# Kernel optimization log

Measured on AMD Instinct MI355X. Metric: run time of the kernel, lower is better.

Reference implementation:

```python
import jax, jax.numpy as jnp
import numpy as np

B, P, N, E, H, D = 8, 1000, 1000, 128, 8, 16  # batch, pomo, nodes, embed, heads, qkv_dim
SQRT_E = float(np.sqrt(E))
CLIP = 10.0
INV_SQRT_D = 1.0 / float(np.sqrt(D))


def _heads(x):
    # [b, n, H*D] -> [b, H, n, D]
    b, n, _ = x.shape
    return x.reshape(b, n, H, D).transpose(0, 2, 1, 3)


def _mha(q, k, v, ninf_mask):
    # q: [b,H,P,D], k/v: [b,H,N,D], ninf_mask: [b,P,N]
    score = jnp.einsum('bhnd,bhsd->bhns', q, k) * INV_SQRT_D
    score = score + ninf_mask[:, None, :, :]
    w = jax.nn.softmax(score, axis=-1)
    out = jnp.einsum('bhns,bhsd->bhnd', w, v)
    return out.transpose(0, 2, 1, 3).reshape(q.shape[0], q.shape[2], H * D)


def setup_inputs() -> dict:
    key = jax.random.key(0)
    ks = jax.random.split(key, 16)
    s = 0.02
    return {
        'encoded_last_node': jax.random.normal(ks[0], (B, P, E), jnp.float32),
        'attr': jax.random.normal(ks[1], (B, P, 4), jnp.float32),
        'encoded_nodes': jax.random.normal(ks[2], (B, N, E), jnp.float32),
        'ninf_mask': jnp.zeros((B, P, N), jnp.float32),
        'Wq_shared': jax.random.normal(ks[3], (E + 4, H * D), jnp.float32) * s,
        'Wk_shared': jax.random.normal(ks[4], (E, H * D), jnp.float32) * s,
        'Wv_shared': jax.random.normal(ks[5], (E, H * D), jnp.float32) * s,
        'Wq_task': jax.random.normal(ks[6], (E + 4, H * D), jnp.float32) * s,
        'Wk_task': jax.random.normal(ks[7], (E, H * D), jnp.float32) * s,
        'Wv_task': jax.random.normal(ks[8], (E, H * D), jnp.float32) * s,
        'Wc_shared': jax.random.normal(ks[9], (H * D, E), jnp.float32) * s,
        'bc_shared': jnp.zeros((E,), jnp.float32),
        'Wc_task': jax.random.normal(ks[10], (H * D, E), jnp.float32) * s,
        'bc_task': jnp.zeros((E,), jnp.float32),
        'Wg': jax.random.normal(ks[11], (E + 4, E), jnp.float32) * s,
        'bg': jnp.zeros((E,), jnp.float32),
    }


def reference(encoded_last_node, attr, encoded_nodes, ninf_mask,
              Wq_shared, Wk_shared, Wv_shared, Wq_task, Wk_task, Wv_task,
              Wc_shared, bc_shared, Wc_task, bc_task, Wg, bg):
    # set_kv
    k_shared = _heads(encoded_nodes @ Wk_shared)
    v_shared = _heads(encoded_nodes @ Wv_shared)
    k_task = _heads(encoded_nodes @ Wk_task)
    v_task = _heads(encoded_nodes @ Wv_task)

    # decoder forward
    input_cat = jnp.concatenate([encoded_last_node, attr], axis=2)  # [B,P,E+4]
    q_shared = _heads(input_cat @ Wq_shared)
    q_task = _heads(input_cat @ Wq_task)

    out_shared = _mha(q_shared, k_shared, v_shared, ninf_mask) @ Wc_shared + bc_shared
    out_task = _mha(q_task, k_task, v_task, ninf_mask) @ Wc_task + bc_task

    gate = jax.nn.sigmoid(input_cat @ Wg + bg)
    gated_out = gate * out_shared + (1.0 - gate) * out_task  # [B,P,E]

    # pointer scores against single-head key (encoded_nodes)
    score = jnp.einsum('bpe,bne->bpn', gated_out, encoded_nodes) / SQRT_E
    score_clipped = CLIP * jnp.tanh(score)
    probs = jax.nn.softmax(score_clipped + ninf_mask, axis=2)
    return probs
```

## Files before the change

### kernel.cpp

```cpp
#include <hip/hip_runtime.h>
#include <math.h>

#define BB 8
#define PP 1000
#define NN 1000
#define EE 128
#define HH 8
#define DD 16

#define INV_SQRT_E 0.08838834764831845f
#define LOG2E      1.4426950408889634f
#define QSCALE     0.3606737602222409f

typedef short short8_t __attribute__((ext_vector_type(8)));
typedef float f32x4    __attribute__((ext_vector_type(4)));
typedef float f32x16   __attribute__((ext_vector_type(16)));
typedef __bf16 bf16x4  __attribute__((ext_vector_type(4)));
typedef __bf16 bf16x8  __attribute__((ext_vector_type(8)));

__device__ __forceinline__ float sigmoid_fast(float x) {
    return 1.f / (1.f + __expf(-x));
}
__device__ __forceinline__ float tanh_fast(float x) {
    x = fminf(fmaxf(x, -15.f), 15.f);
    float e = __expf(2.f * x);
    return (e - 1.f) / (e + 1.f);
}

__device__ __forceinline__ f32x4 mfma16(short8_t a, short8_t b, f32x4 c) {
    return __builtin_amdgcn_mfma_f32_16x16x32_bf16(a, b, c, 0, 0, 0);
}
__device__ __forceinline__ f32x16 mfma32(short8_t a, short8_t b, f32x16 c) {
    return __builtin_amdgcn_mfma_f32_32x32x16_bf16(a, b, c, 0, 0, 0);
}

__device__ __forceinline__ float sum16(float x) {
    int v;
    v = __builtin_amdgcn_update_dpp(0, __builtin_bit_cast(int, x), 0xB1, 0xF, 0xF, true);
    x += __builtin_bit_cast(float, v);
    v = __builtin_amdgcn_update_dpp(0, __builtin_bit_cast(int, x), 0x4E, 0xF, 0xF, true);
    x += __builtin_bit_cast(float, v);
    v = __builtin_amdgcn_update_dpp(0, __builtin_bit_cast(int, x), 0x141, 0xF, 0xF, true);
    x += __builtin_bit_cast(float, v);
    v = __builtin_amdgcn_update_dpp(0, __builtin_bit_cast(int, x), 0x140, 0xF, 0xF, true);
    x += __builtin_bit_cast(float, v);
    return x;
}

__global__ __launch_bounds__(256) void prep_kernel(
    const float* __restrict__ mask, const float* __restrict__ nodes,
    const float* __restrict__ eln,  const float* __restrict__ attr,
    const float* __restrict__ Wk_s, const float* __restrict__ Wv_s,
    const float* __restrict__ Wk_t, const float* __restrict__ Wv_t,
    const float* __restrict__ Wq_s, const float* __restrict__ Wq_t,
    const float* __restrict__ Wg,   const float* __restrict__ Wc_s,
    const float* __restrict__ Wc_t,
    __bf16* __restrict__ emaskb, __bf16* __restrict__ nodesb,
    __bf16* __restrict__ inb, __bf16* __restrict__ Wtb)
{
    const int bx = blockIdx.x;
    __shared__ float tile[32][129];
    if (bx < 7813) {
        int i = (bx * 256 + threadIdx.x) * 4;
        if (i < 8000000) {
            float4 v = *(const float4*)&mask[i];
            bf16x4 pk = { (__bf16)(v.x * LOG2E), (__bf16)(v.y * LOG2E),
                          (__bf16)(v.z * LOG2E), (__bf16)(v.w * LOG2E) };
            *(bf16x4*)&emaskb[i] = pk;
        }
    } else if (bx < 8813) {
        int i = ((bx - 7813) * 256 + threadIdx.x) * 4;
        float4 v = *(const float4*)&nodes[i];
        bf16x4 pk = { (__bf16)v.x, (__bf16)v.y, (__bf16)v.z, (__bf16)v.w };
        *(bf16x4*)&nodesb[i] = pk;
    } else if (bx < 9438) {
        int t = (bx - 8813) * 256 + threadIdx.x;
        int row = t / 20, seg = t - row * 20;
        bf16x8 o = {};
        if (seg < 16) {
            const float* p = &eln[(size_t)row * 128 + seg * 8];
            float4 a = *(const float4*)p, b = *(const float4*)(p + 4);
            o = bf16x8{ (__bf16)a.x, (__bf16)a.y, (__bf16)a.z, (__bf16)a.w,
                        (__bf16)b.x, (__bf16)b.y, (__bf16)b.z, (__bf16)b.w };
        } else if (seg == 16) {
            float4 a = *(const float4*)&attr[(size_t)row * 4];
            o = bf16x8{ (__bf16)a.x, (__bf16)a.y, (__bf16)a.z, (__bf16)a.w,
                        (__bf16)0.f, (__bf16)0.f, (__bf16)0.f, (__bf16)0.f };
        }
        *(bf16x8*)&inb[(size_t)row * 160 + seg * 8] = o;
    } else {
        int idx = bx - 9438;
        int m = idx / 5, kt = idx - m * 5;
        const float* srcs[9] = {Wk_s, Wv_s, Wk_t, Wv_t, Wq_s, Wq_t, Wg, Wc_s, Wc_t};
        const int   srcKs[9] = {128, 128, 128, 128, 132, 132, 132, 128, 128};
        const int   kpads[9] = {128, 128, 128, 128, 160, 160, 160, 128, 128};
        const size_t offs[9] = {0, 16384, 32768, 49152, 65536, 86016, 106496, 126976, 143360};
        const int kp = kpads[m];
        if (kt * 32 >= kp) return;
        const float* src = srcs[m];
        const int sK = srcKs[m];
        const size_t off = offs[m];
        const int tid = threadIdx.x;
        for (int j = tid; j < 32 * 128; j += 256) {
            int kk = j >> 7, n = j & 127;
            int k = kt * 32 + kk;
            tile[kk][n] = (k < sK) ? src[(size_t)k * 128 + n] : 0.f;
        }
        __syncthreads();
        for (int j = tid; j < 32 * 128; j += 256) {
            int n = j >> 5, kk = j & 31;
            Wtb[off + (size_t)n * kp + kt * 32 + kk] = (__bf16)tile[kk][n];
        }
    }
}

template<int NC>
__device__ __forceinline__ void proj_body(
    const __bf16* __restrict__ A, const __bf16* __restrict__ W,
    f32x4 acc[8], int r0, int quad, int lq)
{
    const int K = NC * 32;
    short8_t aF[NC];
    #pragma unroll
    for (int c = 0; c < NC; ++c)
        aF[c] = *(const short8_t*)&A[(size_t)(r0 + lq) * K + c * 32 + quad * 8];
    #pragma unroll
    for (int nt = 0; nt < 8; ++nt) {
        acc[nt] = f32x4{0.f, 0.f, 0.f, 0.f};
        #pragma unroll
        for (int c = 0; c < NC; ++c) {
            short8_t bF = *(const short8_t*)&W[(size_t)(nt * 16 + lq) * K + c * 32 + quad * 8];
            acc[nt] = mfma16(aF[c], bF, acc[nt]);
        }
    }
}

__global__ __launch_bounds__(256) void proj_mfma_kernel(
    const __bf16* __restrict__ nodesb, const __bf16* __restrict__ inb,
    const __bf16* __restrict__ Wtb,
    __bf16* __restrict__ kb_s, __bf16* __restrict__ vt_s,
    __bf16* __restrict__ kb_t, __bf16* __restrict__ vt_t,
    __bf16* __restrict__ qb_s, __bf16* __restrict__ qb_t)
{
    const int wsel = blockIdx.y;
    const int wave = threadIdx.x >> 6, lane = threadIdx.x & 63;
    const int quad = lane >> 4, lq = lane & 15;
    const int r0 = blockIdx.x * 64 + wave * 16;

    f32x4 acc[8];
    if (wsel < 4) {
        proj_body<4>(nodesb, Wtb + (size_t)wsel * 16384, acc, r0, quad, lq);
    } else {
        proj_body<5>(inb, Wtb + 65536 + (size_t)(wsel - 4) * 20480, acc, r0, quad, lq);
    }

    if (wsel == 0 || wsel == 2) {
        __bf16* O = (wsel == 0) ? kb_s : kb_t;
        #pragma unroll
        for (int r = 0; r < 4; ++r) {
            int m = r0 + quad * 4 + r;
            int b = m / 1000, n = m - b * 1000;
            #pragma unroll
            for (int nt = 0; nt < 8; ++nt)
                O[(((size_t)(b * 8 + nt) * 1000 + n) << 4) + lq] = (__bf16)acc[nt][r];
        }
    } else if (wsel == 4 || wsel == 5) {
        __bf16* O = (wsel == 4) ? qb_s : qb_t;
        #pragma unroll
        for (int r = 0; r < 4; ++r) {
            int m = r0 + quad * 4 + r;
            int b = m / 1000, n = m - b * 1000;
            #pragma unroll
            for (int nt = 0; nt < 8; ++nt)
                O[(((size_t)(b * 8 + nt) * 1000 + n) << 4) + lq] =
                    (__bf16)(acc[nt][r] * QSCALE);
        }
    } else {
        __bf16* O = (wsel == 1) ? vt_s : vt_t;
        #pragma unroll
        for (int r = 0; r < 4; ++r) {
            int m = r0 + quad * 4 + r;
            int b = m / 1000, n = m - b * 1000;
            int rr = n & 31;
            int pos = (n & ~31) + ((rr < 16) ? (rr << 1) : (((rr - 16) << 1) | 1));
            #pragma unroll
            for (int nt = 0; nt < 8; ++nt)
                O[(((size_t)(b * 8 + nt) * 16 + lq) << 10) + pos] = (__bf16)acc[nt][r];
        }
    }
}

__global__ __launch_bounds__(256) void attn_mfma_kernel(
    const __bf16* __restrict__ qb_s, const __bf16* __restrict__ qb_t,
    const __bf16* __restrict__ kb_s, const __bf16* __restrict__ kb_t,
    const __bf16* __restrict__ vt_s, const __bf16* __restrict__ vt_t,
    const __bf16* __restrict__ emaskb,
    __bf16* __restrict__ att_s, __bf16* __restrict__ att_t)
{
    const int b    = blockIdx.z;
    const int wave = threadIdx.x >> 6;
    const int combo = blockIdx.y * 4 + wave;
    const int br = combo & 1;
    const int h  = combo >> 1;
    const __bf16* Q  = br ? qb_t : qb_s;
    const __bf16* K  = br ? kb_t : kb_s;
    const __bf16* Vt = br ? vt_t : vt_s;
    __bf16* O        = br ? att_t : att_s;
    const int lane = threadIdx.x & 63;
    const int quad = lane >> 4, lq = lane & 15;
    const int col  = lane & 31;
    const int half = lane >> 5;
    const int bh = b * HH + h;
    const int p0 = blockIdx.x * 32;

    __shared__ __align__(16) __bf16 S[4][2][32][40];

    int pq = p0 + col; if (pq > 999) pq = 999;
    short8_t qB = *(const short8_t*)&Q[(((size_t)bh * 1000 + pq) << 4) + half * 8];

    const __bf16* mp = emaskb + ((size_t)b * 1000 + pq) * 1000 + 4 * half;

    short8_t onesB = { (short)0x3F80, (short)0x3F80, (short)0x3F80, (short)0x3F80,
                       (short)0x3F80, (short)0x3F80, (short)0x3F80, (short)0x3F80 };

    f32x4 o[2] = { {0.f,0.f,0.f,0.f}, {0.f,0.f,0.f,0.f} };
    f32x4 l[2] = { {0.f,0.f,0.f,0.f}, {0.f,0.f,0.f,0.f} };

    short8_t kAc = *(const short8_t*)&K[(((size_t)bh * 1000 + col) << 4) + half * 8];
    short8_t vBc = *(const short8_t*)&Vt[(((size_t)bh * 16 + lq) << 10) + quad * 8];

    #pragma unroll 2
    for (int n0 = 0; n0 < 992; n0 += 32) {
        const int par = (n0 >> 5) & 1;
        int nk = n0 + 32 + col; if (nk > 999) nk = 999;
        short8_t kAn = *(const short8_t*)&K[(((size_t)bh * 1000 + nk) << 4) + half * 8];
        short8_t vBn = *(const short8_t*)&Vt[(((size_t)bh * 16 + lq) << 10) + n0 + 32 + quad * 8];

        bf16x4 m2[4];
        #pragma unroll
        for (int g = 0; g < 4; ++g)
            m2[g] = *(const bf16x4*)&mp[n0 + 8 * g];

        f32x16 s = mfma32(kAc, qB, f32x16{});

        #pragma unroll
        for (int g = 0; g < 4; ++g) {
            bf16x4 pk;
            #pragma unroll
            for (int j = 0; j < 4; ++j)
                pk[j] = (__bf16)__builtin_amdgcn_exp2f(s[4 * g + j] + (float)m2[g][j]);
            *(bf16x4*)&S[wave][par][col][8 * g + 4 * half] = pk;
        }

        #pragma unroll
        for (int t = 0; t < 2; ++t) {
            short8_t aP = *(const short8_t*)&S[wave][par][t * 16 + lq][quad * 8];
            o[t] = mfma16(aP, vBc, o[t]);
            l[t] = mfma16(aP, onesB, l[t]);
        }
        kAc = kAn; vBc = vBn;
    }

    {
        bf16x4 m2t = *(const bf16x4*)&mp[992];
        f32x16 s = mfma32(kAc, qB, f32x16{});

        bf16x4 pk0;
        #pragma unroll
        for (int j = 0; j < 4; ++j)
            pk0[j] = (__bf16)__builtin_amdgcn_exp2f(s[j] + (float)m2t[j]);
        *(bf16x4*)&S[wave][1][col][4 * half] = pk0;
        bf16x4 z = {};
        #pragma unroll
        for (int g = 1; g < 4; ++g)
            *(bf16x4*)&S[wave][1][col][8 * g + 4 * half] = z;

        #pragma unroll
        for (int t = 0; t < 2; ++t) {
            short8_t aP = *(const short8_t*)&S[wave][1][t * 16 + lq][quad * 8];
            o[t] = mfma16(aP, vBc, o[t]);
            l[t] = mfma16(aP, onesB, l[t]);
        }
    }

    #pragma unroll
    for (int t = 0; t < 2; ++t)
        #pragma unroll
        for (int r = 0; r < 4; ++r) {
            int p = p0 + t * 16 + quad * 4 + r;
            if (p < 1000)
                O[((size_t)b * 1000 + p) * 128 + h * 16 + lq] = (__bf16)(o[t][r] / l[t][r]);
        }
}

__global__ __launch_bounds__(128) void combine_mfma_kernel(
    const __bf16* __restrict__ att_s, const __bf16* __restrict__ att_t,
    const __bf16* __restrict__ inb, const __bf16* __restrict__ Wtb,
    const float* __restrict__ bc_s, const float* __restrict__ bc_t,
    const float* __restrict__ bg, __bf16* __restrict__ gatedb)
{
    const int wave = threadIdx.x >> 6, lane = threadIdx.x & 63;
    const int quad = lane >> 4, lq = lane & 15;
    const int r0 = blockIdx.x * 32 + wave * 16;
    const __bf16* Wgp = Wtb + 106496;
    const __bf16* Ws  = Wtb + 126976;
    const __bf16* Wt  = Wtb + 143360;

    short8_t aS[4], aT[4], aG[5];
    #pragma unroll
    for (int c = 0; c < 4; ++c) {
        aS[c] = *(const short8_t*)&att_s[(size_t)(r0 + lq) * 128 + c * 32 + quad * 8];
        aT[c] = *(const short8_t*)&att_t[(size_t)(r0 + lq) * 128 + c * 32 + quad * 8];
    }
    #pragma unroll
    for (int c = 0; c < 5; ++c)
        aG[c] = *(const short8_t*)&inb[(size_t)(r0 + lq) * 160 + c * 32 + quad * 8];

    #pragma unroll
    for (int nt = 0; nt < 8; ++nt) {
        f32x4 accS = {0.f,0.f,0.f,0.f}, accT = accS, accG = accS;
        #pragma unroll
        for (int c = 0; c < 4; ++c) {
            short8_t bS = *(const short8_t*)&Ws[(size_t)(nt * 16 + lq) * 128 + c * 32 + quad * 8];
            short8_t bT = *(const short8_t*)&Wt[(size_t)(nt * 16 + lq) * 128 + c * 32 + quad * 8];
            accS = mfma16(aS[c], bS, accS);
            accT = mfma16(aT[c], bT, accT);
        }
        #pragma unroll
        for (int c = 0; c < 5; ++c) {
            short8_t bG = *(const short8_t*)&Wgp[(size_t)(nt * 16 + lq) * 160 + c * 32 + quad * 8];
            accG = mfma16(aG[c], bG, accG);
        }
        int f = nt * 16 + lq;
        float b1 = bc_s[f], b2 = bc_t[f], b3 = bg[f];
        #pragma unroll
        for (int r = 0; r < 4; ++r) {
            int m = r0 + quad * 4 + r;
            float g = sigmoid_fast(accG[r] + b3);
            float val = g * (accS[r] + b1) + (1.f - g) * (accT[r] + b2);
            gatedb[(size_t)m * 128 + f] = (__bf16)val;
        }
    }
}

__global__ __launch_bounds__(256) void pointer_softmax_kernel(
    const __bf16* __restrict__ gb, const __bf16* __restrict__ nb,
    const __bf16* __restrict__ emaskb, float* __restrict__ out)
{
    const int b    = blockIdx.y;
    const int p0   = blockIdx.x * 16;
    const int wave = threadIdx.x >> 6;
    const int lane = threadIdx.x & 63;
    const int quad = lane >> 4, lq = lane & 15;

    __shared__ float Spart[4][16];

    short8_t aF[4];
    {
        int pp = p0 + lq; if (pp > 999) pp = 999;
        const __bf16* arow = gb + (((size_t)b * 1000 + pp) << 7) + quad * 8;
        #pragma unroll
        for (int kc = 0; kc < 4; ++kc) aF[kc] = *(const short8_t*)&arow[kc * 32];
    }

    float ev[16][4];
    float psum[4] = {0.f, 0.f, 0.f, 0.f};

    #pragma unroll
    for (int i = 0; i < 16; ++i) {
        const int nt = i * 4 + wave;
        const int nn = nt * 16 + lq;
        const bool nv = nn < 1000;
        int nc = nv ? nn : 999;
        const __bf16* brow = nb + (((size_t)b * 1000 + nc) << 7) + quad * 8;
        f32x4 acc = {0.f, 0.f, 0.f, 0.f};
        #pragma unroll
        for (int kc = 0; kc < 4; ++kc) {
            short8_t bF = *(const short8_t*)&brow[kc * 32];
            acc = mfma16(aF[kc], bF, acc);
        }
        #pragma unroll
        for (int r = 0; r < 4; ++r) {
            int p = p0 + quad * 4 + r;
            bool v = nv && (p < 1000);
            size_t midx = v ? ((size_t)b * 1000 + p) * 1000 + nn : 0;
            float m2 = (float)emaskb[midx];
            float sc = 10.f * tanh_fast(acc[r] * INV_SQRT_E);
            float ee = v ? __builtin_amdgcn_exp2f(sc * LOG2E + m2) : 0.f;
            ev[i][r] = ee;
            psum[r] += ee;
        }
    }

    #pragma unroll
    for (int r = 0; r < 4; ++r) psum[r] = sum16(psum[r]);
    if (lq == 0) {
        #pragma unroll
        for (int r = 0; r < 4; ++r) Spart[wave][quad * 4 + r] = psum[r];
    }
    __syncthreads();
    float inv[4];
    #pragma unroll
    for (int r = 0; r < 4; ++r) {
        int row = quad * 4 + r;
        float s = Spart[0][row] + Spart[1][row] + Spart[2][row] + Spart[3][row];
        inv[r] = 1.f / s;
    }

    #pragma unroll
    for (int i = 0; i < 16; ++i) {
        const int nt = i * 4 + wave;
        const int nn = nt * 16 + lq;
        if (nn < 1000) {
            #pragma unroll
            for (int r = 0; r < 4; ++r) {
                int p = p0 + quad * 4 + r;
                if (p < 1000)
                    out[((size_t)b * 1000 + p) * 1000 + nn] = ev[i][r] * inv[r];
            }
        }
    }
}

extern "C" void kernel_launch(void* const* d_in, const int* in_sizes, int n_in,
                              void* d_out, int out_size, void* d_ws, size_t ws_size,
                              hipStream_t stream)
{
    const float* eln   = (const float*)d_in[0];
    const float* attr  = (const float*)d_in[1];
    const float* nodes = (const float*)d_in[2];
    const float* mask  = (const float*)d_in[3];
    const float* Wq_s  = (const float*)d_in[4];
    const float* Wk_s  = (const float*)d_in[5];
    const float* Wv_s  = (const float*)d_in[6];
    const float* Wq_t  = (const float*)d_in[7];
    const float* Wk_t  = (const float*)d_in[8];
    const float* Wv_t  = (const float*)d_in[9];
    const float* Wc_s  = (const float*)d_in[10];
    const float* bc_s  = (const float*)d_in[11];
    const float* Wc_t  = (const float*)d_in[12];
    const float* bc_t  = (const float*)d_in[13];
    const float* Wg    = (const float*)d_in[14];
    const float* bg    = (const float*)d_in[15];
    float* out = (float*)d_out;

    char* w = (char*)d_ws;
    const size_t KB_SZ = (size_t)64 * 1000 * 16 * 2;
    const size_t VT_SZ = (size_t)64 * 16 * 1024 * 2;
    const size_t H_SZ  = (size_t)8000 * 128 * 2;
    const size_t IN_SZ = (size_t)8000 * 160 * 2;
    const size_t EM_SZ = (size_t)8000 * 1000 * 2;
    __bf16* kb_s  = (__bf16*)w;           w += KB_SZ;
    __bf16* kb_t  = (__bf16*)w;           w += KB_SZ;
    __bf16* qb_s  = (__bf16*)w;           w += KB_SZ;
    __bf16* qb_t  = (__bf16*)w;           w += KB_SZ;
    __bf16* vt_s  = (__bf16*)w;           w += VT_SZ;
    __bf16* vt_t  = (__bf16*)w;           w += VT_SZ;
    __bf16* att_s = (__bf16*)w;           w += H_SZ;
    __bf16* att_t = (__bf16*)w;           w += H_SZ;
    __bf16* gatedb = (__bf16*)w;          w += H_SZ;
    __bf16* nodesb = (__bf16*)w;          w += H_SZ;
    __bf16* inb    = (__bf16*)w;          w += IN_SZ;
    __bf16* emaskb = (__bf16*)w;          w += EM_SZ;
    __bf16* Wtb    = (__bf16*)w;          w += 320000;

    hipMemsetAsync(vt_s, 0, 2 * VT_SZ, stream);

    prep_kernel<<<dim3(9483), 256, 0, stream>>>(
        mask, nodes, eln, attr, Wk_s, Wv_s, Wk_t, Wv_t, Wq_s, Wq_t, Wg,
        Wc_s, Wc_t, emaskb, nodesb, inb, Wtb);
    proj_mfma_kernel<<<dim3(125, 6), 256, 0, stream>>>(
        nodesb, inb, Wtb, kb_s, vt_s, kb_t, vt_t, qb_s, qb_t);
    attn_mfma_kernel<<<dim3(32, 4, 8), 256, 0, stream>>>(
        qb_s, qb_t, kb_s, kb_t, vt_s, vt_t, emaskb, att_s, att_t);
    combine_mfma_kernel<<<dim3(250), 128, 0, stream>>>(
        att_s, att_t, inb, Wtb, bc_s, bc_t, bg, gatedb);
    pointer_softmax_kernel<<<dim3(63, 8), 256, 0, stream>>>(
        gatedb, nodesb, emaskb, out);
}
```

Baseline: 228.5 us.

## Retune work decomposition across prep, combine and pointer softmax kernels

```diff
diff --git a/kernel.cpp b/kernel.cpp
--- a/kernel.cpp
+++ b/kernel.cpp
@@ -60,21 +60,42 @@
 {
     const int bx = blockIdx.x;
     __shared__ float tile[32][129];
-    if (bx < 7813) {
-        int i = (bx * 256 + threadIdx.x) * 4;
-        if (i < 8000000) {
-            float4 v = *(const float4*)&mask[i];
-            bf16x4 pk = { (__bf16)(v.x * LOG2E), (__bf16)(v.y * LOG2E),
-                          (__bf16)(v.z * LOG2E), (__bf16)(v.w * LOG2E) };
-            *(bf16x4*)&emaskb[i] = pk;
-        }
-    } else if (bx < 8813) {
-        int i = ((bx - 7813) * 256 + threadIdx.x) * 4;
-        float4 v = *(const float4*)&nodes[i];
-        bf16x4 pk = { (__bf16)v.x, (__bf16)v.y, (__bf16)v.z, (__bf16)v.w };
-        *(bf16x4*)&nodesb[i] = pk;
-    } else if (bx < 9438) {
-        int t = (bx - 8813) * 256 + threadIdx.x;
+    if (bx < 1954) {
+        int base = (bx * 256 + threadIdx.x) * 16;
+        if (base < 8000000) {
+            float4 v0 = *(const float4*)&mask[base];
+            float4 v1 = *(const float4*)&mask[base + 4];
+            float4 v2 = *(const float4*)&mask[base + 8];
+            float4 v3 = *(const float4*)&mask[base + 12];
+            bf16x4 p0 = { (__bf16)(v0.x * LOG2E), (__bf16)(v0.y * LOG2E),
+                          (__bf16)(v0.z * LOG2E), (__bf16)(v0.w * LOG2E) };
+            bf16x4 p1 = { (__bf16)(v1.x * LOG2E), (__bf16)(v1.y * LOG2E),
+                          (__bf16)(v1.z * LOG2E), (__bf16)(v1.w * LOG2E) };
+            bf16x4 p2 = { (__bf16)(v2.x * LOG2E), (__bf16)(v2.y * LOG2E),
+                          (__bf16)(v2.z * LOG2E), (__bf16)(v2.w * LOG2E) };
+            bf16x4 p3 = { (__bf16)(v3.x * LOG2E), (__bf16)(v3.y * LOG2E),
+                          (__bf16)(v3.z * LOG2E), (__bf16)(v3.w * LOG2E) };
+            *(bf16x4*)&emaskb[base]      = p0;
+            *(bf16x4*)&emaskb[base + 4]  = p1;
+            *(bf16x4*)&emaskb[base + 8]  = p2;
+            *(bf16x4*)&emaskb[base + 12] = p3;
+        }
+    } else if (bx < 2204) {
+        int base = ((bx - 1954) * 256 + threadIdx.x) * 16;
+        float4 v0 = *(const float4*)&nodes[base];
+        float4 v1 = *(const float4*)&nodes[base + 4];
+        float4 v2 = *(const float4*)&nodes[base + 8];
+        float4 v3 = *(const float4*)&nodes[base + 12];
+        bf16x4 p0 = { (__bf16)v0.x, (__bf16)v0.y, (__bf16)v0.z, (__bf16)v0.w };
+        bf16x4 p1 = { (__bf16)v1.x, (__bf16)v1.y, (__bf16)v1.z, (__bf16)v1.w };
+        bf16x4 p2 = { (__bf16)v2.x, (__bf16)v2.y, (__bf16)v2.z, (__bf16)v2.w };
+        bf16x4 p3 = { (__bf16)v3.x, (__bf16)v3.y, (__bf16)v3.z, (__bf16)v3.w };
+        *(bf16x4*)&nodesb[base]      = p0;
+        *(bf16x4*)&nodesb[base + 4]  = p1;
+        *(bf16x4*)&nodesb[base + 8]  = p2;
+        *(bf16x4*)&nodesb[base + 12] = p3;
+    } else if (bx < 2829) {
+        int t = (bx - 2204) * 256 + threadIdx.x;
         int row = t / 20, seg = t - row * 20;
         bf16x8 o = {};
         if (seg < 16) {
@@ -89,7 +110,7 @@
         }
         *(bf16x8*)&inb[(size_t)row * 160 + seg * 8] = o;
     } else {
-        int idx = bx - 9438;
+        int idx = bx - 2829;
         int m = idx / 5, kt = idx - m * 5;
         const float* srcs[9] = {Wk_s, Wv_s, Wk_t, Wv_t, Wq_s, Wq_t, Wg, Wc_s, Wc_t};
         const int   srcKs[9] = {128, 128, 128, 128, 132, 132, 132, 128, 128};
@@ -217,7 +238,6 @@
 
     int pq = p0 + col; if (pq > 999) pq = 999;
     short8_t qB = *(const short8_t*)&Q[(((size_t)bh * 1000 + pq) << 4) + half * 8];
-
     const __bf16* mp = emaskb + ((size_t)b * 1000 + pq) * 1000 + 4 * half;
 
     short8_t onesB = { (short)0x3F80, (short)0x3F80, (short)0x3F80, (short)0x3F80,
@@ -235,7 +255,6 @@
         int nk = n0 + 32 + col; if (nk > 999) nk = 999;
         short8_t kAn = *(const short8_t*)&K[(((size_t)bh * 1000 + nk) << 4) + half * 8];
         short8_t vBn = *(const short8_t*)&Vt[(((size_t)bh * 16 + lq) << 10) + n0 + 32 + quad * 8];
-
         bf16x4 m2[4];
         #pragma unroll
         for (int g = 0; g < 4; ++g)
@@ -264,7 +283,6 @@
     {
         bf16x4 m2t = *(const bf16x4*)&mp[992];
         f32x16 s = mfma32(kAc, qB, f32x16{});
-
         bf16x4 pk0;
         #pragma unroll
         for (int j = 0; j < 4; ++j)
@@ -293,7 +311,7 @@
         }
 }
 
-__global__ __launch_bounds__(128) void combine_mfma_kernel(
+__global__ __launch_bounds__(256) void combine_mfma_kernel(
     const __bf16* __restrict__ att_s, const __bf16* __restrict__ att_t,
     const __bf16* __restrict__ inb, const __bf16* __restrict__ Wtb,
     const float* __restrict__ bc_s, const float* __restrict__ bc_t,
@@ -301,7 +319,8 @@
 {
     const int wave = threadIdx.x >> 6, lane = threadIdx.x & 63;
     const int quad = lane >> 4, lq = lane & 15;
-    const int r0 = blockIdx.x * 32 + wave * 16;
+    const int r0 = blockIdx.x * 64 + wave * 16;
+    const int nt = blockIdx.y;
     const __bf16* Wgp = Wtb + 106496;
     const __bf16* Ws  = Wtb + 126976;
     const __bf16* Wt  = Wtb + 143360;
@@ -316,34 +335,31 @@
     for (int c = 0; c < 5; ++c)
         aG[c] = *(const short8_t*)&inb[(size_t)(r0 + lq) * 160 + c * 32 + quad * 8];
 
-    #pragma unroll
-    for (int nt = 0; nt < 8; ++nt) {
-        f32x4 accS = {0.f,0.f,0.f,0.f}, accT = accS, accG = accS;
-        #pragma unroll
-        for (int c = 0; c < 4; ++c) {
-            short8_t bS = *(const short8_t*)&Ws[(size_t)(nt * 16 + lq) * 128 + c * 32 + quad * 8];
-            short8_t bT = *(const short8_t*)&Wt[(size_t)(nt * 16 + lq) * 128 + c * 32 + quad * 8];
-            accS = mfma16(aS[c], bS, accS);
-            accT = mfma16(aT[c], bT, accT);
-        }
-        #pragma unroll
-        for (int c = 0; c < 5; ++c) {
-            short8_t bG = *(const short8_t*)&Wgp[(size_t)(nt * 16 + lq) * 160 + c * 32 + quad * 8];
-            accG = mfma16(aG[c], bG, accG);
-        }
-        int f = nt * 16 + lq;
-        float b1 = bc_s[f], b2 = bc_t[f], b3 = bg[f];
-        #pragma unroll
-        for (int r = 0; r < 4; ++r) {
-            int m = r0 + quad * 4 + r;
-            float g = sigmoid_fast(accG[r] + b3);
-            float val = g * (accS[r] + b1) + (1.f - g) * (accT[r] + b2);
-            gatedb[(size_t)m * 128 + f] = (__bf16)val;
-        }
-    }
-}
-
-__global__ __launch_bounds__(256) void pointer_softmax_kernel(
+    f32x4 accS = {0.f,0.f,0.f,0.f}, accT = accS, accG = accS;
+    #pragma unroll
+    for (int c = 0; c < 4; ++c) {
+        short8_t bS = *(const short8_t*)&Ws[(size_t)(nt * 16 + lq) * 128 + c * 32 + quad * 8];
+        short8_t bT = *(const short8_t*)&Wt[(size_t)(nt * 16 + lq) * 128 + c * 32 + quad * 8];
+        accS = mfma16(aS[c], bS, accS);
+        accT = mfma16(aT[c], bT, accT);
+    }
+    #pragma unroll
+    for (int c = 0; c < 5; ++c) {
+        short8_t bG = *(const short8_t*)&Wgp[(size_t)(nt * 16 + lq) * 160 + c * 32 + quad * 8];
+        accG = mfma16(aG[c], bG, accG);
+    }
+    int f = nt * 16 + lq;
+    float b1 = bc_s[f], b2 = bc_t[f], b3 = bg[f];
+    #pragma unroll
+    for (int r = 0; r < 4; ++r) {
+        int m = r0 + quad * 4 + r;
+        float g = sigmoid_fast(accG[r] + b3);
+        float val = g * (accS[r] + b1) + (1.f - g) * (accT[r] + b2);
+        gatedb[(size_t)m * 128 + f] = (__bf16)val;
+    }
+}
+
+__global__ __launch_bounds__(512) void pointer_softmax_kernel(
     const __bf16* __restrict__ gb, const __bf16* __restrict__ nb,
     const __bf16* __restrict__ emaskb, float* __restrict__ out)
 {
@@ -353,7 +369,7 @@
     const int lane = threadIdx.x & 63;
     const int quad = lane >> 4, lq = lane & 15;
 
-    __shared__ float Spart[4][16];
+    __shared__ float Spart[8][16];
 
     short8_t aF[4];
     {
@@ -363,12 +379,12 @@
         for (int kc = 0; kc < 4; ++kc) aF[kc] = *(const short8_t*)&arow[kc * 32];
     }
 
-    float ev[16][4];
+    float ev[8][4];
     float psum[4] = {0.f, 0.f, 0.f, 0.f};
 
     #pragma unroll
-    for (int i = 0; i < 16; ++i) {
-        const int nt = i * 4 + wave;
+    for (int i = 0; i < 8; ++i) {
+        const int nt = i * 8 + wave;
         const int nn = nt * 16 + lq;
         const bool nv = nn < 1000;
         int nc = nv ? nn : 999;
@@ -403,13 +419,15 @@
     #pragma unroll
     for (int r = 0; r < 4; ++r) {
         int row = quad * 4 + r;
-        float s = Spart[0][row] + Spart[1][row] + Spart[2][row] + Spart[3][row];
+        float s = 0.f;
+        #pragma unroll
+        for (int wv = 0; wv < 8; ++wv) s += Spart[wv][row];
         inv[r] = 1.f / s;
     }
 
     #pragma unroll
-    for (int i = 0; i < 16; ++i) {
-        const int nt = i * 4 + wave;
+    for (int i = 0; i < 8; ++i) {
+        const int nt = i * 8 + wave;
         const int nn = nt * 16 + lq;
         if (nn < 1000) {
             #pragma unroll
@@ -466,15 +484,15 @@
 
     hipMemsetAsync(vt_s, 0, 2 * VT_SZ, stream);
 
-    prep_kernel<<<dim3(9483), 256, 0, stream>>>(
+    prep_kernel<<<dim3(2874), 256, 0, stream>>>(
         mask, nodes, eln, attr, Wk_s, Wv_s, Wk_t, Wv_t, Wq_s, Wq_t, Wg,
         Wc_s, Wc_t, emaskb, nodesb, inb, Wtb);
     proj_mfma_kernel<<<dim3(125, 6), 256, 0, stream>>>(
         nodesb, inb, Wtb, kb_s, vt_s, kb_t, vt_t, qb_s, qb_t);
     attn_mfma_kernel<<<dim3(32, 4, 8), 256, 0, stream>>>(
         qb_s, qb_t, kb_s, kb_t, vt_s, vt_t, emaskb, att_s, att_t);
-    combine_mfma_kernel<<<dim3(250), 128, 0, stream>>>(
+    combine_mfma_kernel<<<dim3(125, 8), 256, 0, stream>>>(
         att_s, att_t, inb, Wtb, bc_s, bc_t, bg, gatedb);
-    pointer_softmax_kernel<<<dim3(63, 8), 256, 0, stream>>>(
+    pointer_softmax_kernel<<<dim3(63, 8), 512, 0, stream>>>(
         gatedb, nodesb, emaskb, out);
 }
```

Result: no change. 228.4 us (-0.0%).
